# Kernel optimization log

Measured on AMD Instinct MI355X. Metric: run time of the kernel, lower is better.

Reference implementation:

```python
import jax, jax.numpy as jnp
import numpy as np


def setup_inputs() -> dict:
    key = jax.random.key(0)
    ks = jax.random.split(key, 7)
    B, Din, H = 65536, 256, 512
    s_in = 1.0 / np.sqrt(Din)
    s_h = 1.0 / np.sqrt(H)
    return {
        "input_x": jax.random.normal(ks[0], (B, Din), jnp.float32),
        "h_old": jax.random.normal(ks[1], (B, H), jnp.float32),
        "c_old": jax.random.normal(ks[2], (B, H), jnp.float32),
        # stacked gate weights, order [i, f, o, c]
        "U": jax.random.normal(ks[3], (4, Din, H), jnp.float32) * s_in,
        "bU": jnp.zeros((4, H), jnp.float32),
        "W": jax.random.normal(ks[4], (4, H, H), jnp.float32) * s_h,
        "bW": jnp.zeros((4, H), jnp.float32),
    }


def reference(input_x, h_old, c_old, U, bU, W, bW):
    # Two fused GEMMs over all four gates: [B, 4, H]
    gx = jnp.einsum('bd,gdh->bgh', input_x, U) + bU[None, :, :]
    gh = jnp.einsum('bh,ghk->bgk', h_old, W) + bW[None, :, :]
    g = gx + gh  # [B, 4, H], gate order i, f, o, c
    i_t = jax.nn.sigmoid(g[:, 0])
    f_t = jax.nn.sigmoid(g[:, 1])
    o_t = jax.nn.sigmoid(g[:, 2])
    c_t = jnp.tanh(g[:, 3])
    c_new = i_t * c_t + f_t * c_old
    h_new = o_t * jnp.tanh(c_new)
    return (h_new, c_new)
```

## Files before the change

kernel.cpp:

```cpp
#include <hip/hip_runtime.h>
#include <stdint.h>
#include <stddef.h>

#define BATCH 65536
#define DIN   256
#define HDIM  512
#define KDIM  768
#define NDIM  2048
#define HN_ELEMS (BATCH * HDIM)

using f32x4 = __attribute__((ext_vector_type(4))) float;
using s16x8 = __attribute__((ext_vector_type(8))) short;
using u16x8 = __attribute__((ext_vector_type(8))) unsigned short;

__device__ __forceinline__ unsigned short f2bf(float f) {
    union { float f; unsigned u; } v; v.f = f;
    unsigned r = v.u + 0x7fffu + ((v.u >> 16) & 1u);
    return (unsigned short)(r >> 16);
}

__global__ __launch_bounds__(256) void pack_a_kernel(
    const float* __restrict__ x, const float* __restrict__ h,
    unsigned short* __restrict__ aPack)
{
    int idx = blockIdx.x * 256 + threadIdx.x;
    int row = idx / 96;
    int seg = idx - row * 96;
    const float* src = (seg < 32) ? (x + (size_t)row * DIN  + seg * 8)
                                  : (h + (size_t)row * HDIM + (seg - 32) * 8);
    const f32x4* s4 = (const f32x4*)src;
    f32x4 v0 = s4[0], v1 = s4[1];
    u16x8 o;
    o[0] = f2bf(v0[0]); o[1] = f2bf(v0[1]); o[2] = f2bf(v0[2]); o[3] = f2bf(v0[3]);
    o[4] = f2bf(v1[0]); o[5] = f2bf(v1[1]); o[6] = f2bf(v1[2]); o[7] = f2bf(v1[3]);
    *(u16x8*)(aPack + (size_t)row * KDIM + seg * 8) = o;
}

__global__ __launch_bounds__(256) void pack_w_kernel(
    const float* __restrict__ U, const float* __restrict__ W,
    unsigned short* __restrict__ wPack)
{
    int idx = blockIdx.x * 256 + threadIdx.x;
    int n = idx / 96;
    int seg = idx - n * 96;
    int k0 = seg * 8;
    int g = (n >> 4) & 3;
    int h = ((n >> 6) << 4) | (n & 15);
    u16x8 o;
    if (k0 < DIN) {
        const float* src = U + ((size_t)g * DIN + k0) * HDIM + h;
#pragma unroll
        for (int kk = 0; kk < 8; ++kk) o[kk] = f2bf(src[(size_t)kk * HDIM]);
    } else {
        const float* src = W + ((size_t)g * HDIM + (k0 - DIN)) * HDIM + h;
#pragma unroll
        for (int kk = 0; kk < 8; ++kk) o[kk] = f2bf(src[(size_t)kk * HDIM]);
    }
    *(u16x8*)(wPack + (size_t)n * KDIM + k0) = o;
}

__global__ __launch_bounds__(256) void pack_bias_kernel(
    const float* __restrict__ bU, const float* __restrict__ bW,
    float* __restrict__ bias)
{
    int n = blockIdx.x * 256 + threadIdx.x;
    int g = (n >> 4) & 3;
    int h = ((n >> 6) << 4) | (n & 15);
    bias[n] = bU[g * HDIM + h] + bW[g * HDIM + h];
}

__global__ __launch_bounds__(256) void lstm_gemm_kernel(
    const unsigned short* __restrict__ aPack,
    const unsigned short* __restrict__ wPack,
    const float* __restrict__ bias,
    const float* __restrict__ c_old,
    float* __restrict__ out)
{
    __shared__ __align__(16) unsigned short smem[8192];

    const int tid = threadIdx.x;
    const int w   = tid >> 6;
    const int l   = tid & 63;
    const int bx  = blockIdx.x;
    const int n0  = (bx & 15) * 128;
    const int m0  = (bx >> 4) * 128;
    const int wm  = w >> 1;
    const int wn  = w & 1;
    const int lq  = l >> 4;
    const int lc  = l & 15;

    const int nbase = n0 + wn * 64;
    const int hcol  = (n0 >> 2) + wn * 16 + lc;
    const float b0 = bias[nbase +  0 + lc];
    const float b1 = bias[nbase + 16 + lc];
    const float b2 = bias[nbase + 32 + lc];
    const float b3 = bias[nbase + 48 + lc];
    float co[4][4];
#pragma unroll
    for (int i = 0; i < 4; ++i)
#pragma unroll
        for (int r = 0; r < 4; ++r)
            co[i][r] = c_old[(size_t)(m0 + wm * 64 + i * 16 + lq * 4 + r) * HDIM + hcol];

    f32x4 acc[4][4];
#pragma unroll
    for (int i = 0; i < 4; ++i)
#pragma unroll
        for (int j = 0; j < 4; ++j)
            acc[i][j] = (f32x4){0.f, 0.f, 0.f, 0.f};

    const int stg_row = w * 16 + (l >> 2);
    const int stg_col = (((l & 3) ^ ((l >> 4) & 3))) * 8;
    const int swz = (lc >> 2) & 3;

    for (int kt = 0; kt < 24; ++kt) {
        const int k0 = kt * 32;
#pragma unroll
        for (int j = 0; j < 2; ++j) {
            const int r = stg_row + j * 64;
            const unsigned short* ga = aPack + (size_t)(m0 + r) * KDIM + k0 + stg_col;
            const unsigned short* gb = wPack + (size_t)(n0 + r) * KDIM + k0 + stg_col;
            unsigned short* la = &smem[(j * 4 + w) * 512];
            unsigned short* lb = &smem[4096 + (j * 4 + w) * 512];
            __builtin_amdgcn_global_load_lds(
                (const __attribute__((address_space(1))) void*)ga,
                (__attribute__((address_space(3))) void*)la, 16, 0, 0);
            __builtin_amdgcn_global_load_lds(
                (const __attribute__((address_space(1))) void*)gb,
                (__attribute__((address_space(3))) void*)lb, 16, 0, 0);
        }
        __syncthreads();

        s16x8 af[4], bf[4];
#pragma unroll
        for (int i = 0; i < 4; ++i) {
            int row = wm * 64 + i * 16 + lc;
            af[i] = *(const s16x8*)&smem[row * 32 + (lq ^ swz) * 8];
        }
#pragma unroll
        for (int j = 0; j < 4; ++j) {
            int row = wn * 64 + j * 16 + lc;
            bf[j] = *(const s16x8*)&smem[4096 + row * 32 + (lq ^ swz) * 8];
        }
#pragma unroll
        for (int i = 0; i < 4; ++i)
#pragma unroll
            for (int j = 0; j < 4; ++j)
                acc[i][j] = __builtin_amdgcn_mfma_f32_16x16x32_bf16(af[i], bf[j], acc[i][j], 0, 0, 0);
        __syncthreads();
    }

    float* fsm  = (float*)smem;
    float* hn_t = fsm;
    float* cn_t = fsm + 1152;

#pragma unroll
    for (int i = 0; i < 4; ++i) {
        f32x4 hnv, cnv;
#pragma unroll
        for (int r = 0; r < 4; ++r) {
            const float gi = acc[i][0][r] + b0;
            const float gf = acc[i][1][r] + b1;
            const float go = acc[i][2][r] + b2;
            const float gc = acc[i][3][r] + b3;
            const float it = 1.f / (1.f + __expf(-gi));
            const float ft = 1.f / (1.f + __expf(-gf));
            const float ot = 1.f / (1.f + __expf(-go));
            const float ct = 2.f / (1.f + __expf(-2.f * gc)) - 1.f;
            const float cn = it * ct + ft * co[i][r];
            const float tc = 2.f / (1.f + __expf(-2.f * cn)) - 1.f;
            cnv[r] = cn;
            hnv[r] = ot * tc;
        }
        __syncthreads();
        {
            const int addr = (wn * 16 + lc) * 36 + wm * 16 + lq * 4;
            *(f32x4*)&hn_t[addr] = hnv;
            *(f32x4*)&cn_t[addr] = cnv;
        }
        __syncthreads();
        {
            const int rloc = tid >> 3;
            const int cg   = tid & 7;
            const int grow = m0 + (rloc >> 4) * 64 + i * 16 + (rloc & 15);
            f32x4 hv, cv;
#pragma unroll
            for (int c = 0; c < 4; ++c) {
                hv[c] = hn_t[(cg * 4 + c) * 36 + rloc];
                cv[c] = cn_t[(cg * 4 + c) * 36 + rloc];
            }
            const size_t ob = (size_t)grow * HDIM + (n0 >> 2) + cg * 4;
            *(f32x4*)&out[ob] = hv;
            *(f32x4*)&out[(size_t)HN_ELEMS + ob] = cv;
        }
    }
}

extern "C" void kernel_launch(void* const* d_in, const int* in_sizes, int n_in,
                              void* d_out, int out_size, void* d_ws, size_t ws_size,
                              hipStream_t stream)
{
    const float* x     = (const float*)d_in[0];
    const float* h_old = (const float*)d_in[1];
    const float* c_old = (const float*)d_in[2];
    const float* U     = (const float*)d_in[3];
    const float* bU    = (const float*)d_in[4];
    const float* W     = (const float*)d_in[5];
    const float* bW    = (const float*)d_in[6];
    float* out = (float*)d_out;

    unsigned short* aPack = (unsigned short*)d_ws;
    unsigned short* wPack = (unsigned short*)((char*)d_ws + (size_t)BATCH * KDIM * 2);
    float* bias = (float*)((char*)wPack + (size_t)NDIM * KDIM * 2);

    pack_a_kernel<<<dim3(24576), dim3(256), 0, stream>>>(x, h_old, aPack);
    pack_w_kernel<<<dim3(768), dim3(256), 0, stream>>>(U, W, wPack);
    pack_bias_kernel<<<dim3(8), dim3(256), 0, stream>>>(bU, bW, bias);
    lstm_gemm_kernel<<<dim3(8192), dim3(256), 0, stream>>>(aPack, wPack, bias, c_old, out);
}
```

Before: 753.1 us.

## Fuse activation bf16 conversion into GEMM with larger double-buffered tiles

Removes the separate pack_a pass. The GEMM kernel now reads x and h_old directly in fp32 and converts them to bf16 in registers with v_cvt_pk_bf16_f32 before writing swizzled LDS. The tile grows to 256x256 with 512 threads and K-step 64, LDS is double-buffered so global loads for the next step overlap the MFMAs, and the block order is remapped to group tiles. This saves writing and re-reading the packed A matrix, at the cost of 128KB of LDS, higher register pressure (8x4 accumulators), and fewer resident blocks.

Result: slower. 887.9 us (+17.9%).

```diff
diff --git a/kernel.cpp b/kernel.cpp
--- a/kernel.cpp
+++ b/kernel.cpp
@@ -12,6 +12,7 @@
 using f32x4 = __attribute__((ext_vector_type(4))) float;
 using s16x8 = __attribute__((ext_vector_type(8))) short;
 using u16x8 = __attribute__((ext_vector_type(8))) unsigned short;
+using u32x4 = __attribute__((ext_vector_type(4))) unsigned int;
 
 __device__ __forceinline__ unsigned short f2bf(float f) {
     union { float f; unsigned u; } v; v.f = f;
@@ -19,21 +20,10 @@
     return (unsigned short)(r >> 16);
 }
 
-__global__ __launch_bounds__(256) void pack_a_kernel(
-    const float* __restrict__ x, const float* __restrict__ h,
-    unsigned short* __restrict__ aPack)
-{
-    int idx = blockIdx.x * 256 + threadIdx.x;
-    int row = idx / 96;
-    int seg = idx - row * 96;
-    const float* src = (seg < 32) ? (x + (size_t)row * DIN  + seg * 8)
-                                  : (h + (size_t)row * HDIM + (seg - 32) * 8);
-    const f32x4* s4 = (const f32x4*)src;
-    f32x4 v0 = s4[0], v1 = s4[1];
-    u16x8 o;
-    o[0] = f2bf(v0[0]); o[1] = f2bf(v0[1]); o[2] = f2bf(v0[2]); o[3] = f2bf(v0[3]);
-    o[4] = f2bf(v1[0]); o[5] = f2bf(v1[1]); o[6] = f2bf(v1[2]); o[7] = f2bf(v1[3]);
-    *(u16x8*)(aPack + (size_t)row * KDIM + seg * 8) = o;
+__device__ __forceinline__ unsigned pk2(float lo, float hi) {
+    unsigned r;
+    asm("v_cvt_pk_bf16_f32 %0, %1, %2" : "=v"(r) : "v"(lo), "v"(hi));
+    return r;
 }
 
 __global__ __launch_bounds__(256) void pack_w_kernel(
@@ -69,93 +59,150 @@
     bias[n] = bU[g * HDIM + h] + bW[g * HDIM + h];
 }
 
-__global__ __launch_bounds__(256) void lstm_gemm_kernel(
-    const unsigned short* __restrict__ aPack,
+__global__ __launch_bounds__(512, 2) void lstm_fused_kernel(
+    const float* __restrict__ x,
+    const float* __restrict__ hOld,
     const unsigned short* __restrict__ wPack,
     const float* __restrict__ bias,
-    const float* __restrict__ c_old,
+    const float* __restrict__ cOld,
     float* __restrict__ out)
 {
-    __shared__ __align__(16) unsigned short smem[8192];
+    __shared__ __align__(16) unsigned short smem[65536];
 
     const int tid = threadIdx.x;
-    const int w   = tid >> 6;
-    const int l   = tid & 63;
-    const int bx  = blockIdx.x;
-    const int n0  = (bx & 15) * 128;
-    const int m0  = (bx >> 4) * 128;
-    const int wm  = w >> 1;
-    const int wn  = w & 1;
-    const int lq  = l >> 4;
-    const int lc  = l & 15;
+    const int w  = tid >> 6;
+    const int l  = tid & 63;
+    const int wm = w >> 2;
+    const int wn = w & 3;
+    const int lq = l >> 4;
+    const int lc = l & 15;
+
+    const int bid = blockIdx.x;
+    const int wg  = (bid & 7) * 256 + (bid >> 3);
+    const int mt  = wg >> 3;
+    const int nt  = wg & 7;
+    const int m0  = mt * 256;
+    const int n0  = nt * 256;
+
+    const int ar = tid >> 1;
+    const int ah = tid & 1;
+    const float* xrow = x    + (size_t)(m0 + ar) * DIN  + ah * 32;
+    const float* hrow = hOld + (size_t)(m0 + ar) * HDIM + ah * 32;
+    const int awsw = ar & 7;
+
+    const int brow   = w * 32 + (l >> 3);
+    const int bchunk = (l & 7) ^ ((l >> 3) & 7);
+    const unsigned short* bsrc = wPack + (size_t)(n0 + brow) * KDIM + bchunk * 8;
+
+    f32x4 acc[8][4];
+#pragma unroll
+    for (int i = 0; i < 8; ++i)
+#pragma unroll
+        for (int j = 0; j < 4; ++j)
+            acc[i][j] = (f32x4){0.f, 0.f, 0.f, 0.f};
+
+    {
+        f32x4 av[8];
+#pragma unroll
+        for (int u = 0; u < 8; ++u) av[u] = ((const f32x4*)xrow)[u];
+#pragma unroll
+        for (int q = 0; q < 4; ++q) {
+            const unsigned short* gb = bsrc + (size_t)q * 8 * KDIM;
+            __builtin_amdgcn_global_load_lds(
+                (const __attribute__((address_space(1))) void*)gb,
+                (__attribute__((address_space(3))) void*)&smem[32768 + (w * 32 + q * 8) * 64],
+                16, 0, 0);
+        }
+#pragma unroll
+        for (int u = 0; u < 4; ++u) {
+            u32x4 o;
+            o[0] = pk2(av[2 * u][0],     av[2 * u][1]);
+            o[1] = pk2(av[2 * u][2],     av[2 * u][3]);
+            o[2] = pk2(av[2 * u + 1][0], av[2 * u + 1][1]);
+            o[3] = pk2(av[2 * u + 1][2], av[2 * u + 1][3]);
+            *(u32x4*)&smem[ar * 64 + (((ah * 4 + u) ^ awsw) << 3)] = o;
+        }
+    }
+    __syncthreads();
+
+#pragma unroll
+    for (int kt = 0; kt < 12; ++kt) {
+        const int cur = kt & 1;
+        const int nxt = cur ^ 1;
+
+        f32x4 av[8];
+        if (kt < 11) {
+            const float* s = (kt + 1 < 4) ? (xrow + (kt + 1) * 64)
+                                          : (hrow + (kt - 3) * 64);
+#pragma unroll
+            for (int u = 0; u < 8; ++u) av[u] = ((const f32x4*)s)[u];
+#pragma unroll
+            for (int q = 0; q < 4; ++q) {
+                const unsigned short* gb = bsrc + (size_t)q * 8 * KDIM + (kt + 1) * 64;
+                __builtin_amdgcn_global_load_lds(
+                    (const __attribute__((address_space(1))) void*)gb,
+                    (__attribute__((address_space(3))) void*)&smem[32768 + nxt * 16384 + (w * 32 + q * 8) * 64],
+                    16, 0, 0);
+            }
+        }
+
+        {
+            const int aoff = cur * 16384 + (wm * 128 + lc) * 64;
+            const int boff = 32768 + cur * 16384 + (wn * 64 + lc) * 64;
+            const int sx = lc & 7;
+#pragma unroll
+            for (int ks = 0; ks < 2; ++ks) {
+                const int slot = (((ks * 4 + lq) ^ sx)) << 3;
+                s16x8 af[8], bf4[4];
+#pragma unroll
+                for (int i = 0; i < 8; ++i)
+                    af[i] = *(const s16x8*)&smem[aoff + i * 1024 + slot];
+#pragma unroll
+                for (int j = 0; j < 4; ++j)
+                    bf4[j] = *(const s16x8*)&smem[boff + j * 1024 + slot];
+#pragma unroll
+                for (int i = 0; i < 8; ++i)
+#pragma unroll
+                    for (int j = 0; j < 4; ++j)
+                        acc[i][j] = __builtin_amdgcn_mfma_f32_16x16x32_bf16(
+                            af[i], bf4[j], acc[i][j], 0, 0, 0);
+            }
+        }
+
+        if (kt < 11) {
+#pragma unroll
+            for (int u = 0; u < 4; ++u) {
+                u32x4 o;
+                o[0] = pk2(av[2 * u][0],     av[2 * u][1]);
+                o[1] = pk2(av[2 * u][2],     av[2 * u][3]);
+                o[2] = pk2(av[2 * u + 1][0], av[2 * u + 1][1]);
+                o[3] = pk2(av[2 * u + 1][2], av[2 * u + 1][3]);
+                *(u32x4*)&smem[nxt * 16384 + ar * 64 + (((ah * 4 + u) ^ awsw) << 3)] = o;
+            }
+        }
+        __syncthreads();
+    }
 
     const int nbase = n0 + wn * 64;
-    const int hcol  = (n0 >> 2) + wn * 16 + lc;
     const float b0 = bias[nbase +  0 + lc];
     const float b1 = bias[nbase + 16 + lc];
     const float b2 = bias[nbase + 32 + lc];
     const float b3 = bias[nbase + 48 + lc];
-    float co[4][4];
-#pragma unroll
-    for (int i = 0; i < 4; ++i)
+    const int hcol = (n0 >> 2) + wn * 16 + lc;
+
+    float co[8][4];
+#pragma unroll
+    for (int i = 0; i < 8; ++i)
 #pragma unroll
         for (int r = 0; r < 4; ++r)
-            co[i][r] = c_old[(size_t)(m0 + wm * 64 + i * 16 + lq * 4 + r) * HDIM + hcol];
-
-    f32x4 acc[4][4];
-#pragma unroll
-    for (int i = 0; i < 4; ++i)
-#pragma unroll
-        for (int j = 0; j < 4; ++j)
-            acc[i][j] = (f32x4){0.f, 0.f, 0.f, 0.f};
-
-    const int stg_row = w * 16 + (l >> 2);
-    const int stg_col = (((l & 3) ^ ((l >> 4) & 3))) * 8;
-    const int swz = (lc >> 2) & 3;
-
-    for (int kt = 0; kt < 24; ++kt) {
-        const int k0 = kt * 32;
-#pragma unroll
-        for (int j = 0; j < 2; ++j) {
-            const int r = stg_row + j * 64;
-            const unsigned short* ga = aPack + (size_t)(m0 + r) * KDIM + k0 + stg_col;
-            const unsigned short* gb = wPack + (size_t)(n0 + r) * KDIM + k0 + stg_col;
-            unsigned short* la = &smem[(j * 4 + w) * 512];
-            unsigned short* lb = &smem[4096 + (j * 4 + w) * 512];
-            __builtin_amdgcn_global_load_lds(
-                (const __attribute__((address_space(1))) void*)ga,
-                (__attribute__((address_space(3))) void*)la, 16, 0, 0);
-            __builtin_amdgcn_global_load_lds(
-                (const __attribute__((address_space(1))) void*)gb,
-                (__attribute__((address_space(3))) void*)lb, 16, 0, 0);
-        }
-        __syncthreads();
-
-        s16x8 af[4], bf[4];
-#pragma unroll
-        for (int i = 0; i < 4; ++i) {
-            int row = wm * 64 + i * 16 + lc;
-            af[i] = *(const s16x8*)&smem[row * 32 + (lq ^ swz) * 8];
-        }
-#pragma unroll
-        for (int j = 0; j < 4; ++j) {
-            int row = wn * 64 + j * 16 + lc;
-            bf[j] = *(const s16x8*)&smem[4096 + row * 32 + (lq ^ swz) * 8];
-        }
-#pragma unroll
-        for (int i = 0; i < 4; ++i)
-#pragma unroll
-            for (int j = 0; j < 4; ++j)
-                acc[i][j] = __builtin_amdgcn_mfma_f32_16x16x32_bf16(af[i], bf[j], acc[i][j], 0, 0, 0);
-        __syncthreads();
-    }
+            co[i][r] = cOld[(size_t)(m0 + wm * 128 + i * 16 + lq * 4 + r) * HDIM + hcol];
 
     float* fsm  = (float*)smem;
     float* hn_t = fsm;
-    float* cn_t = fsm + 1152;
-
-#pragma unroll
-    for (int i = 0; i < 4; ++i) {
+    float* cn_t = fsm + 2304;
+
+#pragma unroll
+    for (int i = 0; i < 8; ++i) {
         f32x4 hnv, cnv;
 #pragma unroll
         for (int r = 0; r < 4; ++r) {
@@ -180,14 +227,14 @@
         }
         __syncthreads();
         {
-            const int rloc = tid >> 3;
-            const int cg   = tid & 7;
-            const int grow = m0 + (rloc >> 4) * 64 + i * 16 + (rloc & 15);
+            const int rl = tid >> 4;
+            const int cg = tid & 15;
+            const int grow = m0 + (rl >> 4) * 128 + i * 16 + (rl & 15);
             f32x4 hv, cv;
 #pragma unroll
             for (int c = 0; c < 4; ++c) {
-                hv[c] = hn_t[(cg * 4 + c) * 36 + rloc];
-                cv[c] = cn_t[(cg * 4 + c) * 36 + rloc];
+                hv[c] = hn_t[(cg * 4 + c) * 36 + rl];
+                cv[c] = cn_t[(cg * 4 + c) * 36 + rl];
             }
             const size_t ob = (size_t)grow * HDIM + (n0 >> 2) + cg * 4;
             *(f32x4*)&out[ob] = hv;
@@ -209,12 +256,10 @@
     const float* bW    = (const float*)d_in[6];
     float* out = (float*)d_out;
 
-    unsigned short* aPack = (unsigned short*)d_ws;
-    unsigned short* wPack = (unsigned short*)((char*)d_ws + (size_t)BATCH * KDIM * 2);
-    float* bias = (float*)((char*)wPack + (size_t)NDIM * KDIM * 2);
-
-    pack_a_kernel<<<dim3(24576), dim3(256), 0, stream>>>(x, h_old, aPack);
+    unsigned short* wPack = (unsigned short*)d_ws;
+    float* bias = (float*)((char*)d_ws + (size_t)NDIM * KDIM * 2);
+
     pack_w_kernel<<<dim3(768), dim3(256), 0, stream>>>(U, W, wPack);
     pack_bias_kernel<<<dim3(8), dim3(256), 0, stream>>>(bU, bW, bias);
-    lstm_gemm_kernel<<<dim3(8192), dim3(256), 0, stream>>>(aPack, wPack, bias, c_old, out);
-}
+    lstm_fused_kernel<<<dim3(2048), dim3(512), 0, stream>>>(x, h_old, wPack, bias, c_old, out);
+}
```

## Fuse fp32-to-bf16 activation packing into GEMM with double-buffered LDS

Applied to the files above, without the earlier changes.

Removes the separate pack_a kernel and the bf16 activation round trip through global memory. The GEMM now loads fp32 x/h_old rows directly, converts them with v_cvt_pk_bf16_f32 into swizzled LDS, and double-buffers both A and B tiles so loads for the next k-step overlap the MFMAs. It also remaps block ids so neighbouring workgroups share tiles and sets a 3-block occupancy hint. The trade-off is that each fp32 A tile is re-read once per N tile (16 times), more LDS, and more register pressure.

Result: slower. 769.8 us (+2.2%).

```diff
diff --git a/kernel.cpp b/kernel.cpp
--- a/kernel.cpp
+++ b/kernel.cpp
@@ -12,6 +12,7 @@
 using f32x4 = __attribute__((ext_vector_type(4))) float;
 using s16x8 = __attribute__((ext_vector_type(8))) short;
 using u16x8 = __attribute__((ext_vector_type(8))) unsigned short;
+using u32x4 = __attribute__((ext_vector_type(4))) unsigned int;
 
 __device__ __forceinline__ unsigned short f2bf(float f) {
     union { float f; unsigned u; } v; v.f = f;
@@ -19,21 +20,10 @@
     return (unsigned short)(r >> 16);
 }
 
-__global__ __launch_bounds__(256) void pack_a_kernel(
-    const float* __restrict__ x, const float* __restrict__ h,
-    unsigned short* __restrict__ aPack)
-{
-    int idx = blockIdx.x * 256 + threadIdx.x;
-    int row = idx / 96;
-    int seg = idx - row * 96;
-    const float* src = (seg < 32) ? (x + (size_t)row * DIN  + seg * 8)
-                                  : (h + (size_t)row * HDIM + (seg - 32) * 8);
-    const f32x4* s4 = (const f32x4*)src;
-    f32x4 v0 = s4[0], v1 = s4[1];
-    u16x8 o;
-    o[0] = f2bf(v0[0]); o[1] = f2bf(v0[1]); o[2] = f2bf(v0[2]); o[3] = f2bf(v0[3]);
-    o[4] = f2bf(v1[0]); o[5] = f2bf(v1[1]); o[6] = f2bf(v1[2]); o[7] = f2bf(v1[3]);
-    *(u16x8*)(aPack + (size_t)row * KDIM + seg * 8) = o;
+__device__ __forceinline__ unsigned pk2(float lo, float hi) {
+    unsigned r;
+    asm("v_cvt_pk_bf16_f32 %0, %1, %2" : "=v"(r) : "v"(lo), "v"(hi));
+    return r;
 }
 
 __global__ __launch_bounds__(256) void pack_w_kernel(
@@ -69,86 +59,140 @@
     bias[n] = bU[g * HDIM + h] + bW[g * HDIM + h];
 }
 
-__global__ __launch_bounds__(256) void lstm_gemm_kernel(
-    const unsigned short* __restrict__ aPack,
+__global__ __launch_bounds__(256, 3) void lstm_fused_kernel(
+    const float* __restrict__ x,
+    const float* __restrict__ hOld,
     const unsigned short* __restrict__ wPack,
     const float* __restrict__ bias,
-    const float* __restrict__ c_old,
+    const float* __restrict__ cOld,
     float* __restrict__ out)
 {
-    __shared__ __align__(16) unsigned short smem[8192];
+    __shared__ __align__(16) unsigned short smem[16384];
 
     const int tid = threadIdx.x;
-    const int w   = tid >> 6;
-    const int l   = tid & 63;
-    const int bx  = blockIdx.x;
-    const int n0  = (bx & 15) * 128;
-    const int m0  = (bx >> 4) * 128;
-    const int wm  = w >> 1;
-    const int wn  = w & 1;
-    const int lq  = l >> 4;
-    const int lc  = l & 15;
+    const int w  = tid >> 6;
+    const int l  = tid & 63;
+    const int wm = w >> 1;
+    const int wn = w & 1;
+    const int lq = l >> 4;
+    const int lc = l & 15;
+
+    const int bid = blockIdx.x;
+    const int wg  = (bid & 7) * 1024 + (bid >> 3);
+    const int nt  = wg & 15;
+    const int mt  = wg >> 4;
+    const int m0  = mt * 128;
+    const int n0  = nt * 128;
+
+    const int ar = tid >> 1;
+    const int ah = tid & 1;
+    const float* xrow = x    + (size_t)(m0 + ar) * DIN  + ah * 16;
+    const float* hrow = hOld + (size_t)(m0 + ar) * HDIM + ah * 16;
+    const int akey = (ar >> 2) & 3;
+    const int as0 = ((ah * 2)     ^ akey) * 8;
+    const int as1 = ((ah * 2 + 1) ^ akey) * 8;
+
+    const int brow_l = l >> 2;
+    const int bchunk = (l & 3) ^ ((l >> 4) & 3);
+    const unsigned short* gb0 = wPack + (size_t)(n0 + w * 16 + brow_l) * KDIM + bchunk * 8;
+    const unsigned short* gb1 = gb0 + (size_t)64 * KDIM;
+
+    const int swz = (lc >> 2) & 3;
+
+    f32x4 acc[4][4];
+#pragma unroll
+    for (int i = 0; i < 4; ++i)
+#pragma unroll
+        for (int j = 0; j < 4; ++j)
+            acc[i][j] = (f32x4){0.f, 0.f, 0.f, 0.f};
+
+    {
+        f32x4 av0 = ((const f32x4*)xrow)[0];
+        f32x4 av1 = ((const f32x4*)xrow)[1];
+        f32x4 av2 = ((const f32x4*)xrow)[2];
+        f32x4 av3 = ((const f32x4*)xrow)[3];
+        __builtin_amdgcn_global_load_lds(
+            (const __attribute__((address_space(1))) void*)gb0,
+            (__attribute__((address_space(3))) void*)&smem[8192 + w * 512], 16, 0, 0);
+        __builtin_amdgcn_global_load_lds(
+            (const __attribute__((address_space(1))) void*)gb1,
+            (__attribute__((address_space(3))) void*)&smem[8192 + 2048 + w * 512], 16, 0, 0);
+        u32x4 o0, o1;
+        o0[0] = pk2(av0[0], av0[1]); o0[1] = pk2(av0[2], av0[3]);
+        o0[2] = pk2(av1[0], av1[1]); o0[3] = pk2(av1[2], av1[3]);
+        o1[0] = pk2(av2[0], av2[1]); o1[1] = pk2(av2[2], av2[3]);
+        o1[2] = pk2(av3[0], av3[1]); o1[3] = pk2(av3[2], av3[3]);
+        *(u32x4*)&smem[ar * 32 + as0] = o0;
+        *(u32x4*)&smem[ar * 32 + as1] = o1;
+    }
+    __syncthreads();
+
+    auto step = [&](int kt, int cur) {
+        const int nxt = cur ^ 1;
+        f32x4 av0, av1, av2, av3;
+        const bool pf = (kt < 23);
+        if (pf) {
+            const int k2 = kt + 1;
+            const float* s = (k2 < 8) ? (xrow + k2 * 32) : (hrow + (k2 - 8) * 32);
+            av0 = ((const f32x4*)s)[0];
+            av1 = ((const f32x4*)s)[1];
+            av2 = ((const f32x4*)s)[2];
+            av3 = ((const f32x4*)s)[3];
+            const int bb = 8192 + nxt * 4096;
+            __builtin_amdgcn_global_load_lds(
+                (const __attribute__((address_space(1))) void*)(gb0 + k2 * 32),
+                (__attribute__((address_space(3))) void*)&smem[bb + w * 512], 16, 0, 0);
+            __builtin_amdgcn_global_load_lds(
+                (const __attribute__((address_space(1))) void*)(gb1 + k2 * 32),
+                (__attribute__((address_space(3))) void*)&smem[bb + 2048 + w * 512], 16, 0, 0);
+        }
+        {
+            const int ab = cur * 4096;
+            const int bb = 8192 + cur * 4096;
+            s16x8 af[4], bf4[4];
+#pragma unroll
+            for (int i = 0; i < 4; ++i)
+                af[i] = *(const s16x8*)&smem[ab + (wm * 64 + i * 16 + lc) * 32 + (lq ^ swz) * 8];
+#pragma unroll
+            for (int j = 0; j < 4; ++j)
+                bf4[j] = *(const s16x8*)&smem[bb + (wn * 64 + j * 16 + lc) * 32 + (lq ^ swz) * 8];
+#pragma unroll
+            for (int i = 0; i < 4; ++i)
+#pragma unroll
+                for (int j = 0; j < 4; ++j)
+                    acc[i][j] = __builtin_amdgcn_mfma_f32_16x16x32_bf16(
+                        af[i], bf4[j], acc[i][j], 0, 0, 0);
+        }
+        if (pf) {
+            u32x4 o0, o1;
+            o0[0] = pk2(av0[0], av0[1]); o0[1] = pk2(av0[2], av0[3]);
+            o0[2] = pk2(av1[0], av1[1]); o0[3] = pk2(av1[2], av1[3]);
+            o1[0] = pk2(av2[0], av2[1]); o1[1] = pk2(av2[2], av2[3]);
+            o1[2] = pk2(av3[0], av3[1]); o1[3] = pk2(av3[2], av3[3]);
+            *(u32x4*)&smem[nxt * 4096 + ar * 32 + as0] = o0;
+            *(u32x4*)&smem[nxt * 4096 + ar * 32 + as1] = o1;
+        }
+        __syncthreads();
+    };
+#pragma unroll 1
+    for (int kt = 0; kt < 24; kt += 2) {
+        step(kt, 0);
+        step(kt + 1, 1);
+    }
 
     const int nbase = n0 + wn * 64;
-    const int hcol  = (n0 >> 2) + wn * 16 + lc;
     const float b0 = bias[nbase +  0 + lc];
     const float b1 = bias[nbase + 16 + lc];
     const float b2 = bias[nbase + 32 + lc];
     const float b3 = bias[nbase + 48 + lc];
+    const int hcol = (n0 >> 2) + wn * 16 + lc;
+
     float co[4][4];
 #pragma unroll
     for (int i = 0; i < 4; ++i)
 #pragma unroll
         for (int r = 0; r < 4; ++r)
-            co[i][r] = c_old[(size_t)(m0 + wm * 64 + i * 16 + lq * 4 + r) * HDIM + hcol];
-
-    f32x4 acc[4][4];
-#pragma unroll
-    for (int i = 0; i < 4; ++i)
-#pragma unroll
-        for (int j = 0; j < 4; ++j)
-            acc[i][j] = (f32x4){0.f, 0.f, 0.f, 0.f};
-
-    const int stg_row = w * 16 + (l >> 2);
-    const int stg_col = (((l & 3) ^ ((l >> 4) & 3))) * 8;
-    const int swz = (lc >> 2) & 3;
-
-    for (int kt = 0; kt < 24; ++kt) {
-        const int k0 = kt * 32;
-#pragma unroll
-        for (int j = 0; j < 2; ++j) {
-            const int r = stg_row + j * 64;
-            const unsigned short* ga = aPack + (size_t)(m0 + r) * KDIM + k0 + stg_col;
-            const unsigned short* gb = wPack + (size_t)(n0 + r) * KDIM + k0 + stg_col;
-            unsigned short* la = &smem[(j * 4 + w) * 512];
-            unsigned short* lb = &smem[4096 + (j * 4 + w) * 512];
-            __builtin_amdgcn_global_load_lds(
-                (const __attribute__((address_space(1))) void*)ga,
-                (__attribute__((address_space(3))) void*)la, 16, 0, 0);
-            __builtin_amdgcn_global_load_lds(
-                (const __attribute__((address_space(1))) void*)gb,
-                (__attribute__((address_space(3))) void*)lb, 16, 0, 0);
-        }
-        __syncthreads();
-
-        s16x8 af[4], bf[4];
-#pragma unroll
-        for (int i = 0; i < 4; ++i) {
-            int row = wm * 64 + i * 16 + lc;
-            af[i] = *(const s16x8*)&smem[row * 32 + (lq ^ swz) * 8];
-        }
-#pragma unroll
-        for (int j = 0; j < 4; ++j) {
-            int row = wn * 64 + j * 16 + lc;
-            bf[j] = *(const s16x8*)&smem[4096 + row * 32 + (lq ^ swz) * 8];
-        }
-#pragma unroll
-        for (int i = 0; i < 4; ++i)
-#pragma unroll
-            for (int j = 0; j < 4; ++j)
-                acc[i][j] = __builtin_amdgcn_mfma_f32_16x16x32_bf16(af[i], bf[j], acc[i][j], 0, 0, 0);
-        __syncthreads();
-    }
+            co[i][r] = cOld[(size_t)(m0 + wm * 64 + i * 16 + lq * 4 + r) * HDIM + hcol];
 
     float* fsm  = (float*)smem;
     float* hn_t = fsm;
@@ -209,12 +253,10 @@
     const float* bW    = (const float*)d_in[6];
     float* out = (float*)d_out;
 
-    unsigned short* aPack = (unsigned short*)d_ws;
-    unsigned short* wPack = (unsigned short*)((char*)d_ws + (size_t)BATCH * KDIM * 2);
-    float* bias = (float*)((char*)wPack + (size_t)NDIM * KDIM * 2);
-
-    pack_a_kernel<<<dim3(24576), dim3(256), 0, stream>>>(x, h_old, aPack);
+    unsigned short* wPack = (unsigned short*)d_ws;
+    float* bias = (float*)((char*)d_ws + (size_t)NDIM * KDIM * 2);
+
     pack_w_kernel<<<dim3(768), dim3(256), 0, stream>>>(U, W, wPack);
     pack_bias_kernel<<<dim3(8), dim3(256), 0, stream>>>(bU, bW, bias);
-    lstm_gemm_kernel<<<dim3(8192), dim3(256), 0, stream>>>(aPack, wPack, bias, c_old, out);
-}
+    lstm_fused_kernel<<<dim3(8192), dim3(256), 0, stream>>>(x, h_old, wPack, bias, c_old, out);
+}
```
